# Kernel optimization log

Hardware: AMD Instinct MI355X
Metric: run time of the kernel (lower is better)

The kernel has to match this reference:

```python
import jax, jax.numpy as jnp
import numpy as np

SIZE = 8
N_CH = 9            # sum of channels in SHAPES [1,2,2,4]
TAU = 0.1           # soft-threshold strength for RA (prox of tau*||.||_1)
ZETA = 0.99         # safeguarding budget fraction
HIDDEN = 256
IN_F = 4 * N_CH * SIZE * SIZE   # 2304
OUT_F = 2 * N_CH * SIZE * SIZE  # 1152


def setup_inputs() -> dict:
    key = jax.random.key(0)
    ks = jax.random.split(key, 8)
    B = 16384
    noisy = jax.random.normal(ks[0], (B, 1, SIZE, SIZE), jnp.float32)
    s1 = 1.0 / np.sqrt(IN_F)
    s2 = 1.0 / np.sqrt(HIDDEN)
    W1 = jax.random.uniform(ks[1], (IN_F, HIDDEN), jnp.float32, -s1, s1)
    b1 = jax.random.uniform(ks[2], (HIDDEN,), jnp.float32, -s1, s1)
    W2 = jax.random.uniform(ks[3], (HIDDEN, HIDDEN), jnp.float32, -s2, s2)
    b2 = jax.random.uniform(ks[4], (HIDDEN,), jnp.float32, -s2, s2)
    # last layer is zero-init in the source; use small random weights so the
    # deviation path carries nontrivial compute (trained-network proxy)
    W3 = 0.01 * jax.random.normal(ks[5], (HIDDEN, OUT_F), jnp.float32)
    b3 = 0.01 * jax.random.normal(ks[6], (OUT_F,), jnp.float32)
    return {"noisy": noisy, "W1": W1, "b1": b1, "W2": W2, "b2": b2,
            "W3": W3, "b3": b3, "T": 20}


def reference(noisy, W1, b1, W2, b2, W3, b3, T):
    B = noisy.shape[0]
    # pack all blocks along channel dim: block0 = noisy, blocks 1..3 = zeros
    x0 = jnp.concatenate(
        [noisy, jnp.zeros((B, N_CH - 1, SIZE, SIZE), noisy.dtype)], axis=1)
    zeros = jnp.zeros_like(x0)

    def mlp(a, b, c, d):  # DeviationNet.forward on packed blocks
        inp = jnp.concatenate([a, b, c, d], axis=1).reshape(B, -1)  # [B, 2304]
        h = jax.nn.relu(inp @ W1 + b1)
        h = jax.nn.relu(h @ W2 + b2)
        out = (h @ W3 + b3).reshape(B, 2 * N_CH, SIZE, SIZE)
        return out[:, :N_CH], out[:, N_CH:]

    def step(carry, n):
        x, y_prev, p_prev, z_prev, u, v = carry
        nf = n.astype(x.dtype)
        # schedule (stand-ins for build_algo_functions): gamma=1, lam=1,
        # alpha(n)=alpha_bar(n)=n/(n+3), theta_bar*beta_bar/theta_hat=1
        gam = 1.0
        a_n = nf / (nf + 3.0)
        ab_n = a_n
        lam = 1.0
        # one_step (all coefficients are scalars, so packed elementwise ops
        # are exactly the per-block list comprehensions)
        y = x + a_n * (y_prev - x) + u
        z = (x + a_n * (p_prev - x) + ab_n * (z_prev - p_prev)
             + gam * u + v)
        Cy = y                                  # C = grad of (1/2)||y||^2
        zm = z - gam * Cy
        pr = jnp.sign(zm) * jnp.maximum(jnp.abs(zm) - gam * TAU, 0.0)  # RA
        x_new = x + lam * (pr - z) + ab_n * lam * (z_prev - p_prev)
        res = jnp.sqrt(jnp.sum((pr - y) ** 2) + 1e-12)
        # compute_delta stand-in: squared update magnitude budget
        delta = jnp.sum((x_new - z) ** 2)
        # DeviationNet on (x_new, p, y, z)
        u_raw, v_raw = mlp(x_new, pr, y, z)
        # SafeguardingLayer: lam(n+1)=1, mu(n+1)=0.5, theta ratios = 1
        lpm = 1.5
        Q = lpm * jnp.sum(u_raw ** 2) + lpm * jnp.sum(v_raw ** 2) + 1e-12
        budget = ZETA * jnp.maximum(delta, 0.0)
        alpha = jnp.sqrt(jnp.minimum(budget / Q, 1.0))
        new_carry = (x_new, y, pr, z, alpha * u_raw, alpha * v_raw)
        return new_carry, res

    carry = (x0, x0, x0, x0, zeros, zeros)
    carry, residuals = jax.lax.scan(step, carry, jnp.arange(T))
    p_final = carry[2]  # p_prev after loop
    return p_final, residuals
```

## Files before the change

### kernel.cpp

```cpp
#include <hip/hip_runtime.h>
#include <math.h>

constexpr int SVEC = 576;
constexpr int INF  = 2304;
constexpr int HID  = 256;
constexpr int OUTF = 1152;
constexpr int TS   = 20;
constexpr int RSL  = 1536;

__device__ __forceinline__ ushort f2bf(float f) {
    union { float f; unsigned u; } a; a.f = f;
    unsigned r = a.u + 0x7fff + ((a.u >> 16) & 1);
    return (ushort)(r >> 16);
}
__device__ __forceinline__ float bf2f(ushort b) {
    union { unsigned u; float f; } a; a.u = ((unsigned)b) << 16;
    return a.f;
}

__device__ __forceinline__ void bar_lgkm() {
    asm volatile("s_waitcnt lgkmcnt(0)\n\ts_barrier" ::: "memory");
}

typedef short  s16x8 __attribute__((ext_vector_type(8)));
typedef float  f32x4 __attribute__((ext_vector_type(4)));

__global__ __launch_bounds__(256) void k_init(ushort* __restrict__ Sb,
                                              const float4* __restrict__ noisy4,
                                              int tot8) {
    int i = blockIdx.x * 256 + threadIdx.x;
    if (i >= tot8) return;
    int sample = i / 288;
    int j = i - sample * 288;
    int jc = j % 72;
    s16x8 o = (s16x8){0,0,0,0,0,0,0,0};
    if (jc < 8) {
        float4 a = noisy4[sample * 16 + jc * 2];
        float4 b = noisy4[sample * 16 + jc * 2 + 1];
        ushort* u = (ushort*)&o;
        u[0]=f2bf(a.x); u[1]=f2bf(a.y); u[2]=f2bf(a.z); u[3]=f2bf(a.w);
        u[4]=f2bf(b.x); u[5]=f2bf(b.y); u[6]=f2bf(b.z); u[7]=f2bf(b.w);
    }
    *(s16x8*)&Sb[(size_t)i * 8] = o;
}

__global__ __launch_bounds__(128) void k_zero(float* __restrict__ p, int n) {
    int i = blockIdx.x * 128 + threadIdx.x;
    if (i < n) p[i] = 0.f;
}

__global__ __launch_bounds__(256) void k_wf(const float* __restrict__ W,
                                            ushort* __restrict__ Wf,
                                            int KS, int stride, int perm,
                                            int total) {
    int o = blockIdx.x * 256 + threadIdx.x;
    if (o >= total) return;
    int e = o & 7;
    int lane = (o >> 3) & 63;
    int rem = o >> 9;
    int s = rem % KS, f = rem / KS;
    int quad = lane >> 4, lm = lane & 15;
    int kp = s * 32 + quad * 8 + e;
    int korig = perm ? (kp & 3) * 576 + (kp >> 2) : kp;
    int n = f * 16 + lm;
    Wf[o] = f2bf(W[(size_t)korig * stride + n]);
}

struct FbsReg { s16x8 x8, p8, y8, z8, u8, v8; };

__device__ __forceinline__ void fbs_load(const ushort* __restrict__ Sb,
                                         const ushort* __restrict__ uv,
                                         size_t sb, size_t ub, FbsReg& f) {
    f.x8 = *(const s16x8*)(Sb + sb);
    f.p8 = *(const s16x8*)(Sb + sb + SVEC);
    f.y8 = *(const s16x8*)(Sb + sb + 2 * SVEC);
    f.z8 = *(const s16x8*)(Sb + sb + 3 * SVEC);
    f.u8 = *(const s16x8*)(uv + ub);
    f.v8 = *(const s16x8*)(uv + ub + SVEC);
}

__device__ __forceinline__ void fbs_finish(ushort* __restrict__ Sb, size_t sb,
                                           ushort* __restrict__ buf,
                                           int frow, int fjg,
                                           float an, float al,
                                           FbsReg& f, float& r, float& d) {
    s16x8 xo, po, yo, zo;
    const ushort* X = (const ushort*)&f.x8; const ushort* P = (const ushort*)&f.p8;
    const ushort* Y = (const ushort*)&f.y8; const ushort* Z = (const ushort*)&f.z8;
    const ushort* U = (const ushort*)&f.u8; const ushort* V = (const ushort*)&f.v8;
    ushort* XO = (ushort*)&xo; ushort* PO = (ushort*)&po;
    ushort* YO = (ushort*)&yo; ushort* ZO = (ushort*)&zo;
    #pragma unroll
    for (int cc = 0; cc < 8; ++cc) {
        float x = bf2f(X[cc]), p = bf2f(P[cc]);
        float yv = bf2f(Y[cc]), zv = bf2f(Z[cc]);
        float u = al * bf2f(U[cc]), v = al * bf2f(V[cc]);
        float y  = x + an * (yv - x) + u;
        float dz = an * (zv - p);
        float z  = x + an * (p - x) + dz + u + v;
        float zm = z - y;
        float t  = fabsf(zm) - 0.1f;
        float pr = (t > 0.f) ? copysignf(t, zm) : 0.f;
        float xn = x + (pr - z) + dz;
        XO[cc] = f2bf(xn); PO[cc] = f2bf(pr); YO[cc] = f2bf(y); ZO[cc] = f2bf(z);
        float e1 = pr - y; r += e1 * e1;
        float e2 = xn - z; d += e2 * e2;
    }
    *(s16x8*)(Sb + sb)            = xo;
    *(s16x8*)(Sb + sb + SVEC)     = po;
    *(s16x8*)(Sb + sb + 2 * SVEC) = yo;
    *(s16x8*)(Sb + sb + 3 * SVEC) = zo;
    #pragma unroll
    for (int cc = 0; cc < 4; ++cc) {
        s16x8 w; ushort* W = (ushort*)&w;
        #pragma unroll
        for (int t = 0; t < 2; ++t) {
            int jj = cc * 2 + t;
            W[t*4+0] = XO[jj]; W[t*4+1] = PO[jj];
            W[t*4+2] = YO[jj]; W[t*4+3] = ZO[jj];
        }
        int ch = (4 * fjg + cc) ^ (frow & 7);
        *(s16x8*)&buf[frow * 256 + ch * 8] = w;
    }
}

__global__ __launch_bounds__(512, 2) void k_step(
    ushort* __restrict__ Sb, ushort* __restrict__ uv,
    const ushort* __restrict__ Wf1, const ushort* __restrict__ Wf2,
    const ushort* __restrict__ Wf3,
    const float* __restrict__ b1v, const float* __restrict__ b2v,
    const float* __restrict__ b3v,
    const float* __restrict__ redprev, float* __restrict__ redcur,
    float an) {
    __shared__ ushort As[2][64 * 256];
    const int tid  = threadIdx.x;
    const int wave = tid >> 6, lane = tid & 63;
    const int lm = lane & 15, quad = lane >> 4;
    const int sample0 = blockIdx.x * 64;
    const int frow = tid >> 3, fjg = tid & 7;

    const s16x8* Wf1v = (const s16x8*)Wf1;
    const s16x8* Wf2v = (const s16x8*)Wf2;
    const s16x8* Wf3v = (const s16x8*)Wf3;

    float av = (lane < 32) ? redprev[512 + lane * 16]
                           : redprev[1024 + (lane - 32) * 16];
    #pragma unroll
    for (int off = 16; off > 0; off >>= 1) av += __shfl_down(av, off);
    const float dsum = __shfl(av, 0), qsum = __shfl(av, 32);
    const float al = sqrtf(fminf(0.99f * fmaxf(dsum, 0.f) /
                                 (1.5f * qsum + 1e-12f), 1.f));

    const size_t srow = (size_t)(sample0 + frow) * INF  + fjg * 8;
    const size_t urow = (size_t)(sample0 + frow) * OUTF + fjg * 8;

    float r = 0.f, d = 0.f;
    FbsReg f;
    s16x8 b1[4][2];

    fbs_load(Sb, uv, srow, urow, f);
    fbs_finish(Sb, srow, As[0], frow, fjg, an, al, f, r, d);
    #pragma unroll
    for (int t = 0; t < 3; ++t)
        #pragma unroll
        for (int j = 0; j < 2; ++j)
            b1[t][j] = Wf1v[((wave * 2 + j) * 72 + t) * 64 + lane];
    bar_lgkm();

    f32x4 acc[4][2];
    #pragma unroll
    for (int i = 0; i < 4; ++i)
        #pragma unroll
        for (int j = 0; j < 2; ++j) acc[i][j] = (f32x4){0.f, 0.f, 0.f, 0.f};

    for (int c = 0; c < 9; ++c) {
        const bool pf = (c < 8);
        const size_t sbn = srow + (size_t)(c + 1) * 64;
        const size_t ubn = urow + (size_t)(c + 1) * 64;
        if (pf) fbs_load(Sb, uv, sbn, ubn, f);
        const ushort* Ab = As[c & 1];
        #pragma unroll
        for (int kk = 0; kk < 8; ++kk) {
            if (c < 8 || kk < 5) {
                const int tg3 = c * 8 + kk + 3;
                #pragma unroll
                for (int j = 0; j < 2; ++j)
                    b1[(kk + 3) & 3][j] =
                        Wf1v[((wave * 2 + j) * 72 + tg3) * 64 + lane];
            }
            s16x8 af[4];
            #pragma unroll
            for (int i = 0; i < 4; ++i)
                af[i] = *(const s16x8*)&Ab[(i * 16 + lm) * 256 +
                         ((((kk << 2) + quad) ^ (lm & 7)) << 3)];
            #pragma unroll
            for (int i = 0; i < 4; ++i)
                #pragma unroll
                for (int j = 0; j < 2; ++j)
                    acc[i][j] = __builtin_amdgcn_mfma_f32_16x16x32_bf16(
                        af[i], b1[kk & 3][j], acc[i][j], 0, 0, 0);
        }
        if (pf) fbs_finish(Sb, sbn, As[(c + 1) & 1], frow, fjg, an, al, f, r, d);
        if (c < 8) bar_lgkm();
    }

    #pragma unroll
    for (int off = 32; off > 0; off >>= 1) {
        r += __shfl_down(r, off);
        d += __shfl_down(d, off);
    }
    if (lane == 0) {
        int bk = ((blockIdx.x << 3) | wave) & 31;
        atomicAdd(&redcur[bk * 16],       r);
        atomicAdd(&redcur[512 + bk * 16], d);
    }

    ushort* h1l = As[1];
    float bb1[2];
    #pragma unroll
    for (int j = 0; j < 2; ++j) bb1[j] = b1v[wave * 32 + j * 16 + lm];
    #pragma unroll
    for (int i = 0; i < 4; ++i)
        #pragma unroll
        for (int j = 0; j < 2; ++j)
            #pragma unroll
            for (int rr = 0; rr < 4; ++rr) {
                int row = i * 16 + quad * 4 + rr;
                int col = wave * 32 + j * 16 + lm;
                float cv = fmaxf(acc[i][j][rr] + bb1[j], 0.f);
                h1l[row * 256 + ((((col >> 3) ^ (row & 7)) << 3) | (col & 7))] =
                    f2bf(cv);
            }
    s16x8 b2[4][2];
    #pragma unroll
    for (int t = 0; t < 3; ++t)
        #pragma unroll
        for (int j = 0; j < 2; ++j)
            b2[t][j] = Wf2v[((wave * 2 + j) * 8 + t) * 64 + lane];
    bar_lgkm();

    f32x4 a2[4][2];
    #pragma unroll
    for (int i = 0; i < 4; ++i)
        #pragma unroll
        for (int j = 0; j < 2; ++j) a2[i][j] = (f32x4){0.f, 0.f, 0.f, 0.f};
    #pragma unroll
    for (int kk = 0; kk < 8; ++kk) {
        if (kk < 5) {
            #pragma unroll
            for (int j = 0; j < 2; ++j)
                b2[(kk + 3) & 3][j] =
                    Wf2v[((wave * 2 + j) * 8 + kk + 3) * 64 + lane];
        }
        s16x8 af[4];
        #pragma unroll
        for (int i = 0; i < 4; ++i)
            af[i] = *(const s16x8*)&h1l[(i * 16 + lm) * 256 +
                     ((((kk << 2) + quad) ^ (lm & 7)) << 3)];
        #pragma unroll
        for (int i = 0; i < 4; ++i)
            #pragma unroll
            for (int j = 0; j < 2; ++j)
                a2[i][j] = __builtin_amdgcn_mfma_f32_16x16x32_bf16(
                    af[i], b2[kk & 3][j], a2[i][j], 0, 0, 0);
    }
    ushort* h2l = As[0];
    float bb2[2];
    #pragma unroll
    for (int j = 0; j < 2; ++j) bb2[j] = b2v[wave * 32 + j * 16 + lm];
    #pragma unroll
    for (int i = 0; i < 4; ++i)
        #pragma unroll
        for (int j = 0; j < 2; ++j)
            #pragma unroll
            for (int rr = 0; rr < 4; ++rr) {
                int row = i * 16 + quad * 4 + rr;
                int col = wave * 32 + j * 16 + lm;
                float cv = fmaxf(a2[i][j][rr] + bb2[j], 0.f);
                h2l[row * 256 + ((((col >> 3) ^ (row & 7)) << 3) | (col & 7))] =
                    f2bf(cv);
            }
    s16x8 b3[4][3];
    #pragma unroll
    for (int t = 0; t < 3; ++t)
        #pragma unroll
        for (int jj = 0; jj < 3; ++jj)
            b3[t][jj] = Wf3v[((wave * 9 + jj) * 8 + t) * 64 + lane];
    bar_lgkm();

    float q = 0.f;
    f32x4 a3[3][4];
    #pragma unroll
    for (int t = 0; t < 24; ++t) {
        const int p = t >> 3, kk = t & 7;
        if (t < 21) {
            const int tp = (t + 3) >> 3, tk = (t + 3) & 7;
            #pragma unroll
            for (int jj = 0; jj < 3; ++jj)
                b3[(t + 3) & 3][jj] =
                    Wf3v[((wave * 9 + tp * 3 + jj) * 8 + tk) * 64 + lane];
        }
        if (kk == 0) {
            #pragma unroll
            for (int jj = 0; jj < 3; ++jj)
                #pragma unroll
                for (int i = 0; i < 4; ++i) a3[jj][i] = (f32x4){0.f,0.f,0.f,0.f};
        }
        s16x8 af[4];
        #pragma unroll
        for (int i = 0; i < 4; ++i)
            af[i] = *(const s16x8*)&h2l[(i * 16 + lm) * 256 +
                     ((((kk << 2) + quad) ^ (lm & 7)) << 3)];
        #pragma unroll
        for (int jj = 0; jj < 3; ++jj)
            #pragma unroll
            for (int i = 0; i < 4; ++i)
                a3[jj][i] = __builtin_amdgcn_mfma_f32_16x16x32_bf16(
                    af[i], b3[t & 3][jj], a3[jj][i], 0, 0, 0);
        if (kk == 7) {
            #pragma unroll
            for (int jj = 0; jj < 3; ++jj) {
                int col = (wave * 9 + p * 3 + jj) * 16 + lm;
                float bb = b3v[col];
                #pragma unroll
                for (int i = 0; i < 4; ++i)
                    #pragma unroll
                    for (int rr = 0; rr < 4; ++rr) {
                        int row = i * 16 + quad * 4 + rr;
                        float cv = a3[jj][i][rr] + bb;
                        q += cv * cv;
                        uv[(size_t)(sample0 + row) * OUTF + col] = f2bf(cv);
                    }
            }
        }
    }
    #pragma unroll
    for (int off = 32; off > 0; off >>= 1) q += __shfl_down(q, off);
    if (lane == 0)
        atomicAdd(&redcur[1024 + (((blockIdx.x << 3) | wave) & 31) * 16], q);
}

__global__ __launch_bounds__(256) void k_finish(const ushort* __restrict__ Sb,
                                                float4* __restrict__ out4,
                                                const float* __restrict__ red,
                                                float* __restrict__ res_out,
                                                int total4 ) {
    int i = blockIdx.x * 256 + threadIdx.x;
    if (blockIdx.x == 0 && threadIdx.x < TS) {
        const float* rb = red + (size_t)(threadIdx.x + 1) * RSL;
        float s = 0.f;
        #pragma unroll
        for (int c = 0; c < 32; ++c) s += rb[c * 16];
        res_out[threadIdx.x] = sqrtf(s + 1e-12f);
    }
    if (i >= total4) return;
    int sample = i / 144;
    int j = i - sample * 144;
    const ushort* p = Sb + (size_t)sample * INF + 576 + j * 4;
    float4 o;
    o.x = bf2f(p[0]); o.y = bf2f(p[1]); o.z = bf2f(p[2]); o.w = bf2f(p[3]);
    out4[i] = o;
}

extern "C" void kernel_launch(void* const* d_in, const int* in_sizes, int n_in,
                              void* d_out, int out_size, void* d_ws, size_t ws_size,
                              hipStream_t stream) {
    const float* noisy = (const float*)d_in[0];
    const float* W1 = (const float*)d_in[1];
    const float* b1 = (const float*)d_in[2];
    const float* W2 = (const float*)d_in[3];
    const float* b2 = (const float*)d_in[4];
    const float* W3 = (const float*)d_in[5];
    const float* b3 = (const float*)d_in[6];
    const int B = in_sizes[0] / 64;

    ushort* Sb  = (ushort*)d_ws;
    ushort* uv  = Sb + (size_t)B * INF;
    ushort* Wf1 = uv + (size_t)B * OUTF;
    ushort* Wf2 = Wf1 + (size_t)HID * INF;
    ushort* Wf3 = Wf2 + (size_t)HID * HID;
    float*  red = (float*)((((uintptr_t)(Wf3 + (size_t)OUTF * HID)) + 63) &
                           ~(uintptr_t)63);

    float* p_out   = (float*)d_out;
    float* res_out = p_out + (size_t)B * SVEC;

    const int tot8S = B * 288;
    const int tot4  = B * 144;

    k_init<<<(tot8S + 255) / 256, 256, 0, stream>>>(Sb, (const float4*)noisy, tot8S);
    k_zero<<<(21 * RSL + 127) / 128, 128, 0, stream>>>(red, 21 * RSL);
    k_wf<<<(HID * INF + 255) / 256, 256, 0, stream>>>(W1, Wf1, 72, HID, 1, HID * INF);
    k_wf<<<(HID * HID + 255) / 256, 256, 0, stream>>>(W2, Wf2, 8, HID, 0, HID * HID);
    k_wf<<<(OUTF * HID + 255) / 256, 256, 0, stream>>>(W3, Wf3, 8, OUTF, 0, OUTF * HID);

    for (int n = 0; n < TS; ++n) {
        float an = (float)n / ((float)n + 3.0f);
        k_step<<<B / 64, 512, 0, stream>>>(Sb, uv, Wf1, Wf2, Wf3, b1, b2, b3,
                                           red + (size_t)n * RSL,
                                           red + (size_t)(n + 1) * RSL, an);
    }
    k_finish<<<(tot4 + 255) / 256, 256, 0, stream>>>(Sb, (float4*)p_out,
                                                     red, res_out, tot4);
}
```

Measured before the change: 1.435 ms.

## Use 16 waves per block and specialize the final step to skip the MLP

```diff
diff --git a/kernel.cpp b/kernel.cpp
--- a/kernel.cpp
+++ b/kernel.cpp
@@ -23,6 +23,7 @@
 }
 
 typedef short  s16x8 __attribute__((ext_vector_type(8)));
+typedef short  s16x4 __attribute__((ext_vector_type(4)));
 typedef float  f32x4 __attribute__((ext_vector_type(4)));
 
 __global__ __launch_bounds__(256) void k_init(ushort* __restrict__ Sb,
@@ -66,17 +67,17 @@
     Wf[o] = f2bf(W[(size_t)korig * stride + n]);
 }
 
-struct FbsReg { s16x8 x8, p8, y8, z8, u8, v8; };
+struct FbsReg { s16x4 x4, p4, y4, z4, u4, v4; };
 
 __device__ __forceinline__ void fbs_load(const ushort* __restrict__ Sb,
                                          const ushort* __restrict__ uv,
                                          size_t sb, size_t ub, FbsReg& f) {
-    f.x8 = *(const s16x8*)(Sb + sb);
-    f.p8 = *(const s16x8*)(Sb + sb + SVEC);
-    f.y8 = *(const s16x8*)(Sb + sb + 2 * SVEC);
-    f.z8 = *(const s16x8*)(Sb + sb + 3 * SVEC);
-    f.u8 = *(const s16x8*)(uv + ub);
-    f.v8 = *(const s16x8*)(uv + ub + SVEC);
+    f.x4 = *(const s16x4*)(Sb + sb);
+    f.p4 = *(const s16x4*)(Sb + sb + SVEC);
+    f.y4 = *(const s16x4*)(Sb + sb + 2 * SVEC);
+    f.z4 = *(const s16x4*)(Sb + sb + 3 * SVEC);
+    f.u4 = *(const s16x4*)(uv + ub);
+    f.v4 = *(const s16x4*)(uv + ub + SVEC);
 }
 
 __device__ __forceinline__ void fbs_finish(ushort* __restrict__ Sb, size_t sb,
@@ -84,14 +85,14 @@
                                            int frow, int fjg,
                                            float an, float al,
                                            FbsReg& f, float& r, float& d) {
-    s16x8 xo, po, yo, zo;
-    const ushort* X = (const ushort*)&f.x8; const ushort* P = (const ushort*)&f.p8;
-    const ushort* Y = (const ushort*)&f.y8; const ushort* Z = (const ushort*)&f.z8;
-    const ushort* U = (const ushort*)&f.u8; const ushort* V = (const ushort*)&f.v8;
+    s16x4 xo, po, yo, zo;
+    const ushort* X = (const ushort*)&f.x4; const ushort* P = (const ushort*)&f.p4;
+    const ushort* Y = (const ushort*)&f.y4; const ushort* Z = (const ushort*)&f.z4;
+    const ushort* U = (const ushort*)&f.u4; const ushort* V = (const ushort*)&f.v4;
     ushort* XO = (ushort*)&xo; ushort* PO = (ushort*)&po;
     ushort* YO = (ushort*)&yo; ushort* ZO = (ushort*)&zo;
     #pragma unroll
-    for (int cc = 0; cc < 8; ++cc) {
+    for (int cc = 0; cc < 4; ++cc) {
         float x = bf2f(X[cc]), p = bf2f(P[cc]);
         float yv = bf2f(Y[cc]), zv = bf2f(Z[cc]);
         float u = al * bf2f(U[cc]), v = al * bf2f(V[cc]);
@@ -106,12 +107,12 @@
         float e1 = pr - y; r += e1 * e1;
         float e2 = xn - z; d += e2 * e2;
     }
-    *(s16x8*)(Sb + sb)            = xo;
-    *(s16x8*)(Sb + sb + SVEC)     = po;
-    *(s16x8*)(Sb + sb + 2 * SVEC) = yo;
-    *(s16x8*)(Sb + sb + 3 * SVEC) = zo;
-    #pragma unroll
-    for (int cc = 0; cc < 4; ++cc) {
+    *(s16x4*)(Sb + sb)            = xo;
+    *(s16x4*)(Sb + sb + SVEC)     = po;
+    *(s16x4*)(Sb + sb + 2 * SVEC) = yo;
+    *(s16x4*)(Sb + sb + 3 * SVEC) = zo;
+    #pragma unroll
+    for (int cc = 0; cc < 2; ++cc) {
         s16x8 w; ushort* W = (ushort*)&w;
         #pragma unroll
         for (int t = 0; t < 2; ++t) {
@@ -119,25 +120,50 @@
             W[t*4+0] = XO[jj]; W[t*4+1] = PO[jj];
             W[t*4+2] = YO[jj]; W[t*4+3] = ZO[jj];
         }
-        int ch = (4 * fjg + cc) ^ (frow & 7);
+        int ch = (2 * fjg + cc) ^ (frow & 7);
         *(s16x8*)&buf[frow * 256 + ch * 8] = w;
     }
 }
 
-__global__ __launch_bounds__(512, 2) void k_step(
+__device__ __forceinline__ void fin_last(float* __restrict__ dst,
+                                         float an, float al,
+                                         FbsReg& f, float& r) {
+    float prf[4];
+    const ushort* X = (const ushort*)&f.x4; const ushort* P = (const ushort*)&f.p4;
+    const ushort* Y = (const ushort*)&f.y4; const ushort* Z = (const ushort*)&f.z4;
+    const ushort* U = (const ushort*)&f.u4; const ushort* V = (const ushort*)&f.v4;
+    #pragma unroll
+    for (int cc = 0; cc < 4; ++cc) {
+        float x = bf2f(X[cc]), p = bf2f(P[cc]);
+        float yv = bf2f(Y[cc]), zv = bf2f(Z[cc]);
+        float u = al * bf2f(U[cc]), v = al * bf2f(V[cc]);
+        float y  = x + an * (yv - x) + u;
+        float dz = an * (zv - p);
+        float z  = x + an * (p - x) + dz + u + v;
+        float zm = z - y;
+        float t  = fabsf(zm) - 0.1f;
+        float pr = (t > 0.f) ? copysignf(t, zm) : 0.f;
+        prf[cc] = pr;
+        float e1 = pr - y; r += e1 * e1;
+    }
+    *(float4*)dst = make_float4(prf[0], prf[1], prf[2], prf[3]);
+}
+
+template<bool LAST>
+__global__ __launch_bounds__(1024) void k_step(
     ushort* __restrict__ Sb, ushort* __restrict__ uv,
     const ushort* __restrict__ Wf1, const ushort* __restrict__ Wf2,
     const ushort* __restrict__ Wf3,
     const float* __restrict__ b1v, const float* __restrict__ b2v,
     const float* __restrict__ b3v,
     const float* __restrict__ redprev, float* __restrict__ redcur,
-    float an) {
+    float an, float* __restrict__ pout) {
     __shared__ ushort As[2][64 * 256];
     const int tid  = threadIdx.x;
     const int wave = tid >> 6, lane = tid & 63;
     const int lm = lane & 15, quad = lane >> 4;
     const int sample0 = blockIdx.x * 64;
-    const int frow = tid >> 3, fjg = tid & 7;
+    const int frow = tid >> 4, fjg = tid & 15;
 
     const s16x8* Wf1v = (const s16x8*)Wf1;
     const s16x8* Wf2v = (const s16x8*)Wf2;
@@ -151,27 +177,52 @@
     const float al = sqrtf(fminf(0.99f * fmaxf(dsum, 0.f) /
                                  (1.5f * qsum + 1e-12f), 1.f));
 
-    const size_t srow = (size_t)(sample0 + frow) * INF  + fjg * 8;
-    const size_t urow = (size_t)(sample0 + frow) * OUTF + fjg * 8;
+    const size_t srow = (size_t)(sample0 + frow) * INF  + fjg * 4;
+    const size_t urow = (size_t)(sample0 + frow) * OUTF + fjg * 4;
 
     float r = 0.f, d = 0.f;
+
+    if constexpr (LAST) {
+        float* prow = pout + (size_t)(sample0 + frow) * SVEC + fjg * 4;
+        FbsReg g0, g1;
+        fbs_load(Sb, uv, srow,      urow,      g0);
+        fbs_load(Sb, uv, srow + 64, urow + 64, g1);
+        fin_last(prow,       an, al, g0, r);
+        fbs_load(Sb, uv, srow + 128, urow + 128, g0);
+        fin_last(prow + 64,  an, al, g1, r);
+        fbs_load(Sb, uv, srow + 192, urow + 192, g1);
+        fin_last(prow + 128, an, al, g0, r);
+        fbs_load(Sb, uv, srow + 256, urow + 256, g0);
+        fin_last(prow + 192, an, al, g1, r);
+        fbs_load(Sb, uv, srow + 320, urow + 320, g1);
+        fin_last(prow + 256, an, al, g0, r);
+        fbs_load(Sb, uv, srow + 384, urow + 384, g0);
+        fin_last(prow + 320, an, al, g1, r);
+        fbs_load(Sb, uv, srow + 448, urow + 448, g1);
+        fin_last(prow + 384, an, al, g0, r);
+        fbs_load(Sb, uv, srow + 512, urow + 512, g0);
+        fin_last(prow + 448, an, al, g1, r);
+        fin_last(prow + 512, an, al, g0, r);
+        #pragma unroll
+        for (int off = 32; off > 0; off >>= 1) r += __shfl_down(r, off);
+        if (lane == 0)
+            atomicAdd(&redcur[(((blockIdx.x << 4) | wave) & 31) * 16], r);
+        return;
+    }
+
     FbsReg f;
-    s16x8 b1[4][2];
+    s16x8 b1[4];
 
     fbs_load(Sb, uv, srow, urow, f);
     fbs_finish(Sb, srow, As[0], frow, fjg, an, al, f, r, d);
     #pragma unroll
     for (int t = 0; t < 3; ++t)
-        #pragma unroll
-        for (int j = 0; j < 2; ++j)
-            b1[t][j] = Wf1v[((wave * 2 + j) * 72 + t) * 64 + lane];
+        b1[t] = Wf1v[((size_t)wave * 72 + t) * 64 + lane];
     bar_lgkm();
 
-    f32x4 acc[4][2];
-    #pragma unroll
-    for (int i = 0; i < 4; ++i)
-        #pragma unroll
-        for (int j = 0; j < 2; ++j) acc[i][j] = (f32x4){0.f, 0.f, 0.f, 0.f};
+    f32x4 acc[4];
+    #pragma unroll
+    for (int i = 0; i < 4; ++i) acc[i] = (f32x4){0.f, 0.f, 0.f, 0.f};
 
     for (int c = 0; c < 9; ++c) {
         const bool pf = (c < 8);
@@ -182,11 +233,8 @@
         #pragma unroll
         for (int kk = 0; kk < 8; ++kk) {
             if (c < 8 || kk < 5) {
-                const int tg3 = c * 8 + kk + 3;
-                #pragma unroll
-                for (int j = 0; j < 2; ++j)
-                    b1[(kk + 3) & 3][j] =
-                        Wf1v[((wave * 2 + j) * 72 + tg3) * 64 + lane];
+                b1[(kk + 3) & 3] =
+                    Wf1v[((size_t)wave * 72 + c * 8 + kk + 3) * 64 + lane];
             }
             s16x8 af[4];
             #pragma unroll
@@ -195,10 +243,8 @@
                          ((((kk << 2) + quad) ^ (lm & 7)) << 3)];
             #pragma unroll
             for (int i = 0; i < 4; ++i)
-                #pragma unroll
-                for (int j = 0; j < 2; ++j)
-                    acc[i][j] = __builtin_amdgcn_mfma_f32_16x16x32_bf16(
-                        af[i], b1[kk & 3][j], acc[i][j], 0, 0, 0);
+                acc[i] = __builtin_amdgcn_mfma_f32_16x16x32_bf16(
+                    af[i], b1[kk & 3], acc[i], 0, 0, 0);
         }
         if (pf) fbs_finish(Sb, sbn, As[(c + 1) & 1], frow, fjg, an, al, f, r, d);
         if (c < 8) bar_lgkm();
@@ -210,48 +256,36 @@
         d += __shfl_down(d, off);
     }
     if (lane == 0) {
-        int bk = ((blockIdx.x << 3) | wave) & 31;
+        int bk = ((blockIdx.x << 4) | wave) & 31;
         atomicAdd(&redcur[bk * 16],       r);
         atomicAdd(&redcur[512 + bk * 16], d);
     }
 
     ushort* h1l = As[1];
-    float bb1[2];
-    #pragma unroll
-    for (int j = 0; j < 2; ++j) bb1[j] = b1v[wave * 32 + j * 16 + lm];
+    const float bb1 = b1v[wave * 16 + lm];
     #pragma unroll
     for (int i = 0; i < 4; ++i)
         #pragma unroll
-        for (int j = 0; j < 2; ++j)
-            #pragma unroll
-            for (int rr = 0; rr < 4; ++rr) {
-                int row = i * 16 + quad * 4 + rr;
-                int col = wave * 32 + j * 16 + lm;
-                float cv = fmaxf(acc[i][j][rr] + bb1[j], 0.f);
-                h1l[row * 256 + ((((col >> 3) ^ (row & 7)) << 3) | (col & 7))] =
-                    f2bf(cv);
-            }
-    s16x8 b2[4][2];
+        for (int rr = 0; rr < 4; ++rr) {
+            int row = i * 16 + quad * 4 + rr;
+            int col = wave * 16 + lm;
+            float cv = fmaxf(acc[i][rr] + bb1, 0.f);
+            h1l[row * 256 + ((((col >> 3) ^ (row & 7)) << 3) | (col & 7))] =
+                f2bf(cv);
+        }
+    s16x8 b2[4];
     #pragma unroll
     for (int t = 0; t < 3; ++t)
-        #pragma unroll
-        for (int j = 0; j < 2; ++j)
-            b2[t][j] = Wf2v[((wave * 2 + j) * 8 + t) * 64 + lane];
+        b2[t] = Wf2v[((size_t)wave * 8 + t) * 64 + lane];
     bar_lgkm();
 
-    f32x4 a2[4][2];
-    #pragma unroll
-    for (int i = 0; i < 4; ++i)
-        #pragma unroll
-        for (int j = 0; j < 2; ++j) a2[i][j] = (f32x4){0.f, 0.f, 0.f, 0.f};
+    f32x4 a2[4];
+    #pragma unroll
+    for (int i = 0; i < 4; ++i) a2[i] = (f32x4){0.f, 0.f, 0.f, 0.f};
     #pragma unroll
     for (int kk = 0; kk < 8; ++kk) {
-        if (kk < 5) {
-            #pragma unroll
-            for (int j = 0; j < 2; ++j)
-                b2[(kk + 3) & 3][j] =
-                    Wf2v[((wave * 2 + j) * 8 + kk + 3) * 64 + lane];
-        }
+        if (kk < 5)
+            b2[(kk + 3) & 3] = Wf2v[((size_t)wave * 8 + kk + 3) * 64 + lane];
         s16x8 af[4];
         #pragma unroll
         for (int i = 0; i < 4; ++i)
@@ -259,75 +293,59 @@
                      ((((kk << 2) + quad) ^ (lm & 7)) << 3)];
         #pragma unroll
         for (int i = 0; i < 4; ++i)
-            #pragma unroll
-            for (int j = 0; j < 2; ++j)
-                a2[i][j] = __builtin_amdgcn_mfma_f32_16x16x32_bf16(
-                    af[i], b2[kk & 3][j], a2[i][j], 0, 0, 0);
+            a2[i] = __builtin_amdgcn_mfma_f32_16x16x32_bf16(
+                af[i], b2[kk & 3], a2[i], 0, 0, 0);
     }
     ushort* h2l = As[0];
-    float bb2[2];
-    #pragma unroll
-    for (int j = 0; j < 2; ++j) bb2[j] = b2v[wave * 32 + j * 16 + lm];
+    const float bb2 = b2v[wave * 16 + lm];
     #pragma unroll
     for (int i = 0; i < 4; ++i)
         #pragma unroll
-        for (int j = 0; j < 2; ++j)
-            #pragma unroll
-            for (int rr = 0; rr < 4; ++rr) {
-                int row = i * 16 + quad * 4 + rr;
-                int col = wave * 32 + j * 16 + lm;
-                float cv = fmaxf(a2[i][j][rr] + bb2[j], 0.f);
-                h2l[row * 256 + ((((col >> 3) ^ (row & 7)) << 3) | (col & 7))] =
-                    f2bf(cv);
+        for (int rr = 0; rr < 4; ++rr) {
+            int row = i * 16 + quad * 4 + rr;
+            int col = wave * 16 + lm;
+            float cv = fmaxf(a2[i][rr] + bb2, 0.f);
+            h2l[row * 256 + ((((col >> 3) ^ (row & 7)) << 3) | (col & 7))] =
+                f2bf(cv);
+        }
+    s16x8 b3[4];
+    #pragma unroll
+    for (int t = 0; t < 3; ++t)
+        b3[t] = Wf3v[((size_t)wave * 8 + t) * 64 + lane];
+    bar_lgkm();
+
+    float q = 0.f;
+    f32x4 a3[4];
+    #pragma unroll
+    for (int t = 0; t < 40; ++t) {
+        const int p = t >> 3, kk = t & 7;
+        const bool act = (p < 4) || (wave < 8);
+        if (act) {
+            const int t3 = t + 3, tp = t3 >> 3, tk = t3 & 7;
+            if (t3 < 40 && (tp < 4 || wave < 8))
+                b3[t3 & 3] = Wf3v[(((size_t)(wave + 16 * tp)) * 8 + tk) * 64 + lane];
+            if (kk == 0) {
+                #pragma unroll
+                for (int i = 0; i < 4; ++i) a3[i] = (f32x4){0.f,0.f,0.f,0.f};
             }
-    s16x8 b3[4][3];
-    #pragma unroll
-    for (int t = 0; t < 3; ++t)
-        #pragma unroll
-        for (int jj = 0; jj < 3; ++jj)
-            b3[t][jj] = Wf3v[((wave * 9 + jj) * 8 + t) * 64 + lane];
-    bar_lgkm();
-
-    float q = 0.f;
-    f32x4 a3[3][4];
-    #pragma unroll
-    for (int t = 0; t < 24; ++t) {
-        const int p = t >> 3, kk = t & 7;
-        if (t < 21) {
-            const int tp = (t + 3) >> 3, tk = (t + 3) & 7;
-            #pragma unroll
-            for (int jj = 0; jj < 3; ++jj)
-                b3[(t + 3) & 3][jj] =
-                    Wf3v[((wave * 9 + tp * 3 + jj) * 8 + tk) * 64 + lane];
-        }
-        if (kk == 0) {
-            #pragma unroll
-            for (int jj = 0; jj < 3; ++jj)
-                #pragma unroll
-                for (int i = 0; i < 4; ++i) a3[jj][i] = (f32x4){0.f,0.f,0.f,0.f};
-        }
-        s16x8 af[4];
-        #pragma unroll
-        for (int i = 0; i < 4; ++i)
-            af[i] = *(const s16x8*)&h2l[(i * 16 + lm) * 256 +
-                     ((((kk << 2) + quad) ^ (lm & 7)) << 3)];
-        #pragma unroll
-        for (int jj = 0; jj < 3; ++jj)
+            s16x8 af[4];
             #pragma unroll
             for (int i = 0; i < 4; ++i)
-                a3[jj][i] = __builtin_amdgcn_mfma_f32_16x16x32_bf16(
-                    af[i], b3[t & 3][jj], a3[jj][i], 0, 0, 0);
-        if (kk == 7) {
+                af[i] = *(const s16x8*)&h2l[(i * 16 + lm) * 256 +
+                         ((((kk << 2) + quad) ^ (lm & 7)) << 3)];
             #pragma unroll
-            for (int jj = 0; jj < 3; ++jj) {
-                int col = (wave * 9 + p * 3 + jj) * 16 + lm;
-                float bb = b3v[col];
+            for (int i = 0; i < 4; ++i)
+                a3[i] = __builtin_amdgcn_mfma_f32_16x16x32_bf16(
+                    af[i], b3[t & 3], a3[i], 0, 0, 0);
+            if (kk == 7) {
+                const int col = (wave + 16 * p) * 16 + lm;
+                const float bb = b3v[col];
                 #pragma unroll
                 for (int i = 0; i < 4; ++i)
                     #pragma unroll
                     for (int rr = 0; rr < 4; ++rr) {
                         int row = i * 16 + quad * 4 + rr;
-                        float cv = a3[jj][i][rr] + bb;
+                        float cv = a3[i][rr] + bb;
                         q += cv * cv;
                         uv[(size_t)(sample0 + row) * OUTF + col] = f2bf(cv);
                     }
@@ -337,29 +355,18 @@
     #pragma unroll
     for (int off = 32; off > 0; off >>= 1) q += __shfl_down(q, off);
     if (lane == 0)
-        atomicAdd(&redcur[1024 + (((blockIdx.x << 3) | wave) & 31) * 16], q);
-}
-
-__global__ __launch_bounds__(256) void k_finish(const ushort* __restrict__ Sb,
-                                                float4* __restrict__ out4,
-                                                const float* __restrict__ red,
-                                                float* __restrict__ res_out,
-                                                int total4 ) {
-    int i = blockIdx.x * 256 + threadIdx.x;
-    if (blockIdx.x == 0 && threadIdx.x < TS) {
-        const float* rb = red + (size_t)(threadIdx.x + 1) * RSL;
-        float s = 0.f;
-        #pragma unroll
-        for (int c = 0; c < 32; ++c) s += rb[c * 16];
-        res_out[threadIdx.x] = sqrtf(s + 1e-12f);
-    }
-    if (i >= total4) return;
-    int sample = i / 144;
-    int j = i - sample * 144;
-    const ushort* p = Sb + (size_t)sample * INF + 576 + j * 4;
-    float4 o;
-    o.x = bf2f(p[0]); o.y = bf2f(p[1]); o.z = bf2f(p[2]); o.w = bf2f(p[3]);
-    out4[i] = o;
+        atomicAdd(&redcur[1024 + (((blockIdx.x << 4) | wave) & 31) * 16], q);
+}
+
+__global__ __launch_bounds__(64) void k_res(const float* __restrict__ red,
+                                            float* __restrict__ res_out) {
+    int t = threadIdx.x;
+    if (t >= TS) return;
+    const float* rb = red + (size_t)(t + 1) * RSL;
+    float s = 0.f;
+    #pragma unroll
+    for (int c = 0; c < 32; ++c) s += rb[c * 16];
+    res_out[t] = sqrtf(s + 1e-12f);
 }
 
 extern "C" void kernel_launch(void* const* d_in, const int* in_sizes, int n_in,
@@ -386,7 +393,6 @@
     float* res_out = p_out + (size_t)B * SVEC;
 
     const int tot8S = B * 288;
-    const int tot4  = B * 144;
 
     k_init<<<(tot8S + 255) / 256, 256, 0, stream>>>(Sb, (const float4*)noisy, tot8S);
     k_zero<<<(21 * RSL + 127) / 128, 128, 0, stream>>>(red, 21 * RSL);
@@ -394,12 +400,17 @@
     k_wf<<<(HID * HID + 255) / 256, 256, 0, stream>>>(W2, Wf2, 8, HID, 0, HID * HID);
     k_wf<<<(OUTF * HID + 255) / 256, 256, 0, stream>>>(W3, Wf3, 8, OUTF, 0, OUTF * HID);
 
-    for (int n = 0; n < TS; ++n) {
+    for (int n = 0; n < TS - 1; ++n) {
         float an = (float)n / ((float)n + 3.0f);
-        k_step<<<B / 64, 512, 0, stream>>>(Sb, uv, Wf1, Wf2, Wf3, b1, b2, b3,
-                                           red + (size_t)n * RSL,
-                                           red + (size_t)(n + 1) * RSL, an);
-    }
-    k_finish<<<(tot4 + 255) / 256, 256, 0, stream>>>(Sb, (float4*)p_out,
-                                                     red, res_out, tot4);
-}
+        k_step<false><<<B / 64, 1024, 0, stream>>>(
+            Sb, uv, Wf1, Wf2, Wf3, b1, b2, b3,
+            red + (size_t)n * RSL, red + (size_t)(n + 1) * RSL, an, p_out);
+    }
+    {
+        float an = (float)(TS - 1) / ((float)(TS - 1) + 3.0f);
+        k_step<true><<<B / 64, 1024, 0, stream>>>(
+            Sb, uv, Wf1, Wf2, Wf3, b1, b2, b3,
+            red + (size_t)(TS - 1) * RSL, red + (size_t)TS * RSL, an, p_out);
+    }
+    k_res<<<1, 64, 0, stream>>>(red, res_out);
+}
```

Result: slower. 1.471 ms (+2.5%).
